# Kernel optimization log

Measured on AMD Instinct MI355X. Metric: run time of the kernel, lower is better.

## Reference

```python
import jax, jax.numpy as jnp
import numpy as np

HEADS = 8
NEG = -1e9
EPS = 1e-9


def setup_inputs() -> dict:
    key = jax.random.key(0)
    ks = jax.random.split(key, 24)
    N, D, E = 2048, 512, 64
    s = 0.02
    inp = {
        "xyz": jax.random.normal(ks[0], (N, 3), jnp.float32),
        "str_feat": jax.random.normal(ks[1], (N, D), jnp.float32),
        "esm_feat": jax.random.normal(ks[2], (N, E), jnp.float32),
        "y_hat": jax.random.uniform(ks[3], (N, 1), jnp.float32),
        "distance_mask": jax.random.randint(ks[4], (N, N), 0, 2, jnp.int32),
        "t": jnp.ones((1,), jnp.float32),
        "band_width": jnp.ones((1,), jnp.float32),
        "max_iter": 5,
        # main projections (torch Linear layout: y = x @ W.T + b)
        "Wq": jax.random.normal(ks[5], (D, D), jnp.float32) * s,
        "bq": jnp.zeros((D,), jnp.float32),
        "Wk": jax.random.normal(ks[6], (D, D), jnp.float32) * s,
        "bk": jnp.zeros((D,), jnp.float32),
        "Wv": jax.random.normal(ks[7], (D, D), jnp.float32) * s,
        "bv": jnp.zeros((D,), jnp.float32),
        "Wo": jax.random.normal(ks[8], (D, D), jnp.float32) * s,
        "bo": jnp.zeros((D,), jnp.float32),
        # esm projections (computed in the original forward but unused downstream)
        "Weq": jax.random.normal(ks[9], (E, E), jnp.float32) * s,
        "beq": jnp.zeros((E,), jnp.float32),
        "Wek": jax.random.normal(ks[10], (E, E), jnp.float32) * s,
        "bek": jnp.zeros((E,), jnp.float32),
        "Wev": jax.random.normal(ks[11], (E, E), jnp.float32) * s,
        "bev": jnp.zeros((E,), jnp.float32),
        "Weo": jax.random.normal(ks[12], (E, E), jnp.float32) * s,
        "beo": jnp.zeros((E,), jnp.float32),
    }
    return inp


def reference(xyz, str_feat, esm_feat, y_hat, distance_mask, t, band_width, max_iter,
              Wq, bq, Wk, bk, Wv, bv, Wo, bo,
              Weq, beq, Wek, bek, Wev, bev, Weo, beo):
    N, D = str_feat.shape
    h = HEADS
    dh = D // h

    q = str_feat @ Wq.T + bq
    k = str_feat @ Wk.T + bk
    v = str_feat @ Wv.T + bv
    # esm projections: computed in the original forward but never used (dead code; DCE'd under jit)
    _esm_q = esm_feat @ Weq.T + beq
    _esm_k = esm_feat @ Wek.T + bek
    _esm_v = esm_feat @ Wev.T + bev

    # [h, N, dh]
    qh = q.reshape(N, h, dh).transpose(1, 0, 2)
    kh = k.reshape(N, h, dh).transpose(1, 0, 2)
    vh = v.reshape(N, h, dh).transpose(1, 0, 2)

    scores = jnp.einsum('hnd,hmd->hnm', qh, kh) / jnp.sqrt(jnp.asarray(dh, qh.dtype))
    mask = (distance_mask > 0)[None]              # [1, N, N]
    yw = y_hat[:, 0][None, :]                     # [1, N] per-target weight
    inv_two_bw2 = 1.0 / (2.0 * band_width[0] ** 2)
    temp = t[0]

    def step(carry, _):
        xyz_c, _x = carry
        # squared pairwise distances via the expanded form (avoids [N,N,3])
        sq = jnp.sum(xyz_c * xyz_c, axis=-1)
        d2 = sq[:, None] + sq[None, :] - 2.0 * (xyz_c @ xyz_c.T)
        kern = jnp.exp(-d2 * inv_two_bw2)          # [N, N] band-width kernel
        logits = scores / temp + jnp.log(kern * yw + EPS)[None]
        logits = jnp.where(mask, logits, NEG)
        attn = jax.nn.softmax(logits, axis=-1)     # [h, N, N]
        xyz_new = jnp.einsum('nm,md->nd', attn.mean(0), xyz_c)  # mean-shift step
        x_new = jnp.einsum('hnm,hmd->hnd', attn, vh)            # [h, N, dh]
        return (xyz_new, x_new), None

    (xyz_out, xh), _ = jax.lax.scan(step, (xyz, jnp.zeros_like(vh)), None, length=max_iter)
    x = xh.transpose(1, 0, 2).reshape(N, D)
    out = x @ Wo.T + bo
    return xyz_out, out
```

## Files before the change

kernel.cpp:

```cpp
#include <hip/hip_runtime.h>


typedef __attribute__((ext_vector_type(8))) short bf16x8;
typedef __attribute__((ext_vector_type(4))) float f32x4;

__device__ __forceinline__ unsigned short f2bf(float f) {
    unsigned int u = __float_as_uint(f);
    u += 0x7fff + ((u >> 16) & 1);
    return (unsigned short)(u >> 16);
}
__device__ __forceinline__ float bf2f(unsigned short u) {
    return __uint_as_float((unsigned int)u << 16);
}

union EU { bf16x8 v; unsigned short u[8]; };

__global__ __launch_bounds__(256)
void conv_all(const float* __restrict__ strf,
              const float* __restrict__ Wq, const float* __restrict__ Wk,
              const float* __restrict__ Wv,
              unsigned short* __restrict__ sA, unsigned short* __restrict__ sW)
{
    const long base = (long)(blockIdx.x * 256 + threadIdx.x) * 8;
    const float* src;
    unsigned short* dst;
    if (base < 1048576) {
        src = strf + base; dst = sA + base;
    } else {
        const long rel = base - 1048576;
        const int seg = (int)(rel >> 18);
        const long off = rel & 262143;
        src = (seg == 0 ? Wq : (seg == 1 ? Wk : Wv)) + off;
        dst = sW + (long)seg * 262144 + off;
    }
    float4 a = *reinterpret_cast<const float4*>(src);
    float4 b = *reinterpret_cast<const float4*>(src + 4);
    EU o;
    o.u[0] = f2bf(a.x); o.u[1] = f2bf(a.y); o.u[2] = f2bf(a.z); o.u[3] = f2bf(a.w);
    o.u[4] = f2bf(b.x); o.u[5] = f2bf(b.y); o.u[6] = f2bf(b.z); o.u[7] = f2bf(b.w);
    *reinterpret_cast<bf16x8*>(dst) = o.v;
}

__global__ __launch_bounds__(256)
void qkv_mfma(const unsigned short* __restrict__ sA,
              const unsigned short* __restrict__ sW,
              const float* __restrict__ bq, const float* __restrict__ bk,
              const float* __restrict__ bv,
              unsigned short* __restrict__ qh, unsigned short* __restrict__ kh,
              unsigned short* __restrict__ vT)
{
    const int z  = blockIdx.z;
    const int bx = blockIdx.x;
    const int by = blockIdx.y;
    const int tid = threadIdx.x;
    const int wv = tid >> 6;
    const int lane = tid & 63;
    const int row  = lane & 15;
    const int koct = (lane >> 4) * 8;
    const int n0 = bx * 64;

    const unsigned short* Ap = sA + (long)(n0 + wv * 16 + row) * 512;
    const unsigned short* Bp = sW + (long)z * 262144 + (long)(by * 64 + row) * 512;

    f32x4 acc[4] = {};
#pragma unroll
    for (int k0 = 0; k0 < 512; k0 += 32) {
        bf16x8 a = *reinterpret_cast<const bf16x8*>(Ap + k0 + koct);
#pragma unroll
        for (int t = 0; t < 4; t++) {
            bf16x8 b = *reinterpret_cast<const bf16x8*>(Bp + (long)(t * 16) * 512 + k0 + koct);
            acc[t] = __builtin_amdgcn_mfma_f32_16x16x32_bf16(a, b, acc[t], 0, 0, 0);
        }
    }

    if (z == 2) {
        const int rbase = n0 + wv * 16 + (lane >> 4) * 4;
#pragma unroll
        for (int t = 0; t < 4; t++) {
            const int d = by * 64 + t * 16 + (lane & 15);
            const float bb = bv[d];
            ushort4 o;
            o.x = f2bf(acc[t][0] + bb); o.y = f2bf(acc[t][1] + bb);
            o.z = f2bf(acc[t][2] + bb); o.w = f2bf(acc[t][3] + bb);
            *reinterpret_cast<ushort4*>(vT + (long)d * 2048 + rbase) = o;
        }
        return;
    }

    __shared__ float ls[64][68];
    const int lrb = wv * 16 + (lane >> 4) * 4;
    const int lcb = lane & 15;
#pragma unroll
    for (int t = 0; t < 4; t++)
#pragma unroll
        for (int r = 0; r < 4; r++)
            ls[lrb + r][t * 16 + lcb] = acc[t][r];
    __syncthreads();

    const float* bias = (z == 0) ? bq : bk;
    unsigned short* dst = (z == 0) ? qh : kh;
    const int r2 = tid >> 2;
    const int c2 = (tid & 3) * 16;
    float sv[16];
#pragma unroll
    for (int j = 0; j < 4; j++) {
        float4 s = *reinterpret_cast<const float4*>(&ls[r2][c2 + j * 4]);
        float4 bb = *reinterpret_cast<const float4*>(bias + by * 64 + c2 + j * 4);
        sv[j*4+0] = s.x + bb.x; sv[j*4+1] = s.y + bb.y;
        sv[j*4+2] = s.z + bb.z; sv[j*4+3] = s.w + bb.w;
    }
    EU o0, o1;
#pragma unroll
    for (int j = 0; j < 8; j++) { o0.u[j] = f2bf(sv[j]); o1.u[j] = f2bf(sv[8 + j]); }
    unsigned short* dp = dst + (long)(n0 + r2) * 512 + by * 64 + c2;
    *reinterpret_cast<bf16x8*>(dp)     = o0.v;
    *reinterpret_cast<bf16x8*>(dp + 8) = o1.v;
}

__global__ __launch_bounds__(256)
void scores_mfma(const unsigned short* __restrict__ qh,
                 const unsigned short* __restrict__ kh,
                 const int* __restrict__ dmask,
                 const float* __restrict__ tptr,
                 unsigned short* __restrict__ Ebf)
{
    const int h  = blockIdx.z;
    const int m0 = blockIdx.x * 128;
    const int n0 = blockIdx.y * 64;
    const int tid = threadIdx.x;
    const int wv = tid >> 6;
    const int lane = tid & 63;
    const float scale = 1.0f / (8.0f * tptr[0]);

    const int row  = lane & 15;
    const int koct = (lane >> 4) * 8;
    const unsigned short* Aq = qh + (long)(n0 + wv * 16 + row) * 512 + h * 64;
    const unsigned short* Bk = kh + (long)(m0 + row) * 512 + h * 64;

    f32x4 acc[8] = {};
#pragma unroll
    for (int k0 = 0; k0 < 64; k0 += 32) {
        bf16x8 a = *reinterpret_cast<const bf16x8*>(Aq + k0 + koct);
#pragma unroll
        for (int t = 0; t < 8; t++) {
            bf16x8 b = *reinterpret_cast<const bf16x8*>(Bk + (long)(t * 16) * 512 + k0 + koct);
            acc[t] = __builtin_amdgcn_mfma_f32_16x16x32_bf16(a, b, acc[t], 0, 0, 0);
        }
    }

    __shared__ float ls[64][68];
    const int lrb = wv * 16 + (lane >> 4) * 4;
    const int lcb = lane & 15;
    const int r2 = tid >> 2;
    const int c2 = (tid & 3) * 16;
    const int gn = n0 + r2;

#pragma unroll
    for (int half = 0; half < 2; half++) {
#pragma unroll
        for (int t = 0; t < 4; t++)
#pragma unroll
            for (int r = 0; r < 4; r++)
                ls[lrb + r][t * 16 + lcb] = acc[half * 4 + t][r];
        __syncthreads();

        const int mcol = m0 + half * 64 + c2;
        const int* mp = dmask + (long)gn * 2048 + mcol;
        int4 mk0 = reinterpret_cast<const int4*>(mp)[0];
        int4 mk1 = reinterpret_cast<const int4*>(mp)[1];
        int4 mk2 = reinterpret_cast<const int4*>(mp)[2];
        int4 mk3 = reinterpret_cast<const int4*>(mp)[3];
        int mk[16] = {mk0.x, mk0.y, mk0.z, mk0.w, mk1.x, mk1.y, mk1.z, mk1.w,
                      mk2.x, mk2.y, mk2.z, mk2.w, mk3.x, mk3.y, mk3.z, mk3.w};
        float4 s0 = *reinterpret_cast<const float4*>(&ls[r2][c2 + 0]);
        float4 s1 = *reinterpret_cast<const float4*>(&ls[r2][c2 + 4]);
        float4 s2 = *reinterpret_cast<const float4*>(&ls[r2][c2 + 8]);
        float4 s3 = *reinterpret_cast<const float4*>(&ls[r2][c2 + 12]);
        float sv[16] = {s0.x, s0.y, s0.z, s0.w, s1.x, s1.y, s1.z, s1.w,
                        s2.x, s2.y, s2.z, s2.w, s3.x, s3.y, s3.z, s3.w};
        EU o0, o1;
#pragma unroll
        for (int j = 0; j < 8; j++)
            o0.u[j] = (mk[j] > 0) ? f2bf(__expf(sv[j] * scale)) : (unsigned short)0;
#pragma unroll
        for (int j = 0; j < 8; j++)
            o1.u[j] = (mk[8 + j] > 0) ? f2bf(__expf(sv[8 + j] * scale)) : (unsigned short)0;
        unsigned short* ep = Ebf + (long)gn * 16384 + h * 2048 + mcol;
        *reinterpret_cast<bf16x8*>(ep)     = o0.v;
        *reinterpret_cast<bf16x8*>(ep + 8) = o1.v;
        __syncthreads();
    }
}

__global__ __launch_bounds__(256)
void ms_iter(const unsigned short* __restrict__ Ebf,
             const float* __restrict__ xyz_src,
             float* __restrict__ xyz_dst,
             const float* __restrict__ y_hat,
             const float* __restrict__ bwp,
             unsigned short* __restrict__ attn_out,
             int write_attn)
{
    const int n = blockIdx.x;
    const int tid = threadIdx.x;
    const int lane = tid & 63;
    const int wave = tid >> 6;
    const int m0 = tid * 8;

    __shared__ float red[64];

    const float bw = bwp[0];
    const float c2k = 1.0f / (2.0f * bw * bw);

    const float xn = xyz_src[n * 3 + 0];
    const float yn = xyz_src[n * 3 + 1];
    const float zn = xyz_src[n * 3 + 2];
    const float sqn = xn * xn + yn * yn + zn * zn;

    float mx[8], my[8], mz[8];
    {
        const float4* xp = reinterpret_cast<const float4*>(xyz_src + (long)m0 * 3);
        float4 a = xp[0], b = xp[1], c = xp[2], d = xp[3], e = xp[4], f = xp[5];
        mx[0]=a.x; my[0]=a.y; mz[0]=a.z;  mx[1]=a.w; my[1]=b.x; mz[1]=b.y;
        mx[2]=b.z; my[2]=b.w; mz[2]=c.x;  mx[3]=c.y; my[3]=c.z; mz[3]=c.w;
        mx[4]=d.x; my[4]=d.y; mz[4]=d.z;  mx[5]=d.w; my[5]=e.x; mz[5]=e.y;
        mx[6]=e.z; my[6]=e.w; mz[6]=f.x;  mx[7]=f.y; my[7]=f.z; mz[7]=f.w;
    }
    float4 yh0 = *reinterpret_cast<const float4*>(y_hat + m0);
    float4 yh1 = *reinterpret_cast<const float4*>(y_hat + m0 + 4);
    float yh[8] = {yh0.x, yh0.y, yh0.z, yh0.w, yh1.x, yh1.y, yh1.z, yh1.w};

    float g[8];
#pragma unroll
    for (int j = 0; j < 8; j++) {
        const float d2 = sqn + (mx[j]*mx[j] + my[j]*my[j] + mz[j]*mz[j])
                       - 2.0f * (xn*mx[j] + yn*my[j] + zn*mz[j]);
        g[j] = __expf(-d2 * c2k) * yh[j] + 1e-9f;
    }

    const unsigned short* Ep = Ebf + (long)n * 16384 + m0;
    EU E[8];
#pragma unroll
    for (int h = 0; h < 8; h++)
        E[h].v = *reinterpret_cast<const bf16x8*>(Ep + h * 2048);

    float z[8];
#pragma unroll
    for (int h = 0; h < 8; h++) {
        float zz = 0.f;
#pragma unroll
        for (int j = 0; j < 8; j++) zz += bf2f(E[h].u[j]) * g[j];
        z[h] = zz;
    }

#pragma unroll
    for (int h = 0; h < 8; h++) {
        float v = z[h];
#pragma unroll
        for (int off = 32; off > 0; off >>= 1) v += __shfl_down(v, off, 64);
        if (lane == 0) red[wave * 8 + h] = v;
    }
    __syncthreads();
    if (tid < 8) {
        const float s = red[tid] + red[8 + tid] + red[16 + tid] + red[24 + tid];
        red[32 + tid] = 1.0f / s;
    }
    __syncthreads();
    float invz[8];
#pragma unroll
    for (int h = 0; h < 8; h++) invz[h] = red[32 + h];
    __syncthreads();

    float ax = 0.f, ay = 0.f, az = 0.f;
#pragma unroll
    for (int j = 0; j < 8; j++) {
        float w = 0.f;
#pragma unroll
        for (int h = 0; h < 8; h++) w += bf2f(E[h].u[j]) * invz[h];
        w *= 0.125f * g[j];
        ax += w * mx[j]; ay += w * my[j]; az += w * mz[j];
    }
    if (write_attn) {
        unsigned short* ap = attn_out + (long)n * 16384 + m0;
#pragma unroll
        for (int h = 0; h < 8; h++) {
            EU o;
#pragma unroll
            for (int j = 0; j < 8; j++)
                o.u[j] = f2bf(bf2f(E[h].u[j]) * g[j] * invz[h]);
            *reinterpret_cast<bf16x8*>(ap + h * 2048) = o.v;
        }
    }

    float v3[3] = {ax, ay, az};
#pragma unroll
    for (int c = 0; c < 3; c++) {
        float v = v3[c];
#pragma unroll
        for (int off = 32; off > 0; off >>= 1) v += __shfl_down(v, off, 64);
        if (lane == 0) red[c * 4 + wave] = v;
    }
    __syncthreads();
    if (tid < 3) {
        xyz_dst[n * 3 + tid] = red[tid * 4 + 0] + red[tid * 4 + 1] +
                               red[tid * 4 + 2] + red[tid * 4 + 3];
    }
}

__global__ __launch_bounds__(256)
void av_mfma(const unsigned short* __restrict__ attn,
             const unsigned short* __restrict__ vT,
             float* __restrict__ xb)
{
    const int h  = blockIdx.z;
    const int s  = blockIdx.y;
    const int bx = blockIdx.x;
    const int wv = threadIdx.x >> 6;
    const int lane = threadIdx.x & 63;
    const int n0 = bx * 64 + wv * 16;
    const int kc = s * 512;

    const int mrow = lane & 15;
    const int koct = (lane >> 4) * 8;

    const unsigned short* Ab = attn + (long)(n0 + mrow) * 16384 + h * 2048;
    const unsigned short* Bb = vT + ((long)h * 64 + mrow) * 2048;

    f32x4 acc[4] = {};
    for (int k0 = kc; k0 < kc + 512; k0 += 32) {
        bf16x8 a = *reinterpret_cast<const bf16x8*>(Ab + k0 + koct);
#pragma unroll
        for (int t = 0; t < 4; t++) {
            bf16x8 b = *reinterpret_cast<const bf16x8*>(Bb + (long)(t * 16) * 2048 + k0 + koct);
            acc[t] = __builtin_amdgcn_mfma_f32_16x16x32_bf16(a, b, acc[t], 0, 0, 0);
        }
    }

    const int rbase = n0 + (lane >> 4) * 4;
    const int dcol = lane & 15;
#pragma unroll
    for (int t = 0; t < 4; t++)
#pragma unroll
        for (int r = 0; r < 4; r++)
            atomicAdd(&xb[(long)(rbase + r) * 512 + h * 64 + t * 16 + dcol], acc[t][r]);
}

__global__ __launch_bounds__(256)
void gemm_nt(const float* __restrict__ A,
             const float* __restrict__ B,
             const float* __restrict__ bias,
             float* __restrict__ C)
{
    __shared__ float As[16][68];
    __shared__ float Bs[16][68];

    const int tid = threadIdx.x;
    const int i0 = blockIdx.x * 64;
    const int j0 = blockIdx.y * 64;
    const int tx = tid & 15, ty = tid >> 4;
    const int lr = tid >> 2;
    const int lc = (tid & 3) << 2;

    float acc[4][4] = {};

    for (int k0 = 0; k0 < 512; k0 += 16) {
        float4 av = *reinterpret_cast<const float4*>(A + (long)(i0 + lr) * 512 + (k0 + lc));
        float4 bv = *reinterpret_cast<const float4*>(B + (long)(j0 + lr) * 512 + (k0 + lc));
        As[lc + 0][lr] = av.x; As[lc + 1][lr] = av.y; As[lc + 2][lr] = av.z; As[lc + 3][lr] = av.w;
        Bs[lc + 0][lr] = bv.x; Bs[lc + 1][lr] = bv.y; Bs[lc + 2][lr] = bv.z; Bs[lc + 3][lr] = bv.w;
        __syncthreads();
#pragma unroll
        for (int kk = 0; kk < 16; kk++) {
            float4 a = *reinterpret_cast<const float4*>(&As[kk][ty << 2]);
            float4 b = *reinterpret_cast<const float4*>(&Bs[kk][tx << 2]);
            float ar[4] = {a.x, a.y, a.z, a.w};
            float br[4] = {b.x, b.y, b.z, b.w};
#pragma unroll
            for (int p = 0; p < 4; p++)
#pragma unroll
                for (int q = 0; q < 4; q++)
                    acc[p][q] += ar[p] * br[q];
        }
        __syncthreads();
    }

#pragma unroll
    for (int p = 0; p < 4; p++) {
        const int row = i0 + (ty << 2) + p;
        const int col = j0 + (tx << 2);
        float4 o;
        o.x = acc[p][0] + bias[col + 0];
        o.y = acc[p][1] + bias[col + 1];
        o.z = acc[p][2] + bias[col + 2];
        o.w = acc[p][3] + bias[col + 3];
        *reinterpret_cast<float4*>(C + (long)row * 512 + col) = o;
    }
}

extern "C" void kernel_launch(void* const* d_in, const int* in_sizes, int n_in,
                              void* d_out, int out_size, void* d_ws, size_t ws_size,
                              hipStream_t stream)
{
    (void)in_sizes; (void)n_in; (void)out_size; (void)ws_size;

    const float* xyz   = (const float*)d_in[0];
    const float* strf  = (const float*)d_in[1];
    const float* yhat  = (const float*)d_in[3];
    const int*   dmask = (const int*)d_in[4];
    const float* tptr  = (const float*)d_in[5];
    const float* bwptr = (const float*)d_in[6];
    const float* Wq = (const float*)d_in[8];
    const float* bq = (const float*)d_in[9];
    const float* Wk = (const float*)d_in[10];
    const float* bk = (const float*)d_in[11];
    const float* Wv = (const float*)d_in[12];
    const float* bv = (const float*)d_in[13];
    const float* Wo = (const float*)d_in[14];
    const float* bo = (const float*)d_in[15];
    float* outp = (float*)d_out;

    char* wsb = (char*)d_ws;
    float* xb            = (float*)(wsb);
    unsigned short* sA   = (unsigned short*)(wsb + (4L << 20));
    unsigned short* sW   = (unsigned short*)(wsb + (6L << 20));
    unsigned short* qh   = (unsigned short*)(wsb + (8L << 20));
    unsigned short* kh   = (unsigned short*)(wsb + (10L << 20));
    unsigned short* vT   = (unsigned short*)(wsb + (12L << 20));
    float* xyzA          = (float*)(wsb + (14L << 20));
    float* xyzB          = xyzA + 8192;
    unsigned short* Ebf  = (unsigned short*)(wsb + (16L << 20));

    dim3 blk(256, 1, 1);

    conv_all<<<dim3(896), blk, 0, stream>>>(strf, Wq, Wk, Wv, sA, sW);
    qkv_mfma<<<dim3(32, 8, 3), blk, 0, stream>>>(sA, sW, bq, bk, bv, qh, kh, vT);

    scores_mfma<<<dim3(16, 32, 8), blk, 0, stream>>>(qh, kh, dmask, tptr, Ebf);

    const float* src = xyz;
    float* dsts[5] = {xyzA, xyzB, xyzA, xyzB, outp};
    for (int it = 0; it < 5; it++) {
        ms_iter<<<dim3(2048), blk, 0, stream>>>(Ebf, src, dsts[it], yhat, bwptr,
                                                Ebf, it == 4 ? 1 : 0);
        src = dsts[it];
    }

    hipMemsetAsync(xb, 0, 2048L * 512 * sizeof(float), stream);
    av_mfma<<<dim3(32, 4, 8), blk, 0, stream>>>(Ebf, vT, xb);

    gemm_nt<<<dim3(32, 8, 1), blk, 0, stream>>>(xb, Wo, bo, outp + 6144);
}
```

Before: 372.2 us.

## Pack distance mask to bytes once and streamline scores epilogue with per-wave LDS

The conversion kernel now also packs the int32 distance mask into a byte mask, so scores_mfma reads 4x less mask data across its 8 head passes. The scores epilogue drops the block-wide LDS staging and two barriers: each wave writes exp'd bf16 values to its own LDS tile, then applies the byte mask and stores 32 contiguous elements per lane. The E loads in ms_iter are hoisted to the top and made nontemporal, and av_mfma's attention loads are also nontemporal. In exchange, an extra 4MB pass over the mask is added to the conversion launch and extra workspace is used.

```diff
diff --git a/kernel.cpp b/kernel.cpp
--- a/kernel.cpp
+++ b/kernel.cpp
@@ -2,7 +2,9 @@
 
 
 typedef __attribute__((ext_vector_type(8))) short bf16x8;
+typedef __attribute__((ext_vector_type(4))) short bf16x4;
 typedef __attribute__((ext_vector_type(4))) float f32x4;
+typedef __attribute__((ext_vector_type(4))) int   i32x4;
 
 __device__ __forceinline__ unsigned short f2bf(float f) {
     unsigned int u = __float_as_uint(f);
@@ -13,15 +15,29 @@
     return __uint_as_float((unsigned int)u << 16);
 }
 
-union EU { bf16x8 v; unsigned short u[8]; };
+union EU  { bf16x8 v; i32x4 i; unsigned short u[8]; };
+union EU4 { bf16x4 v; unsigned short u[4]; };
 
 __global__ __launch_bounds__(256)
 void conv_all(const float* __restrict__ strf,
               const float* __restrict__ Wq, const float* __restrict__ Wk,
-              const float* __restrict__ Wv,
-              unsigned short* __restrict__ sA, unsigned short* __restrict__ sW)
+              const float* __restrict__ Wv, const int* __restrict__ dmask,
+              unsigned short* __restrict__ sA, unsigned short* __restrict__ sW,
+              unsigned char* __restrict__ mby)
 {
     const long base = (long)(blockIdx.x * 256 + threadIdx.x) * 8;
+    if (base >= 1048576 + 786432) {
+        const long rel = base - (1048576 + 786432);
+        int4 a = *reinterpret_cast<const int4*>(dmask + rel);
+        int4 b = *reinterpret_cast<const int4*>(dmask + rel + 4);
+        unsigned long long p = 0;
+        p |= (a.x > 0) ? 0x01ULL : 0;  p |= (a.y > 0) ? 0x0100ULL : 0;
+        p |= (a.z > 0) ? 0x010000ULL : 0;  p |= (a.w > 0) ? 0x01000000ULL : 0;
+        p |= (b.x > 0) ? 0x0100000000ULL : 0;  p |= (b.y > 0) ? 0x010000000000ULL : 0;
+        p |= (b.z > 0) ? 0x01000000000000ULL : 0;  p |= (b.w > 0) ? 0x0100000000000000ULL : 0;
+        *reinterpret_cast<unsigned long long*>(mby + rel) = p;
+        return;
+    }
     const float* src;
     unsigned short* dst;
     if (base < 1048576) {
@@ -120,7 +136,7 @@
 __global__ __launch_bounds__(256)
 void scores_mfma(const unsigned short* __restrict__ qh,
                  const unsigned short* __restrict__ kh,
-                 const int* __restrict__ dmask,
+                 const unsigned char* __restrict__ mby,
                  const float* __restrict__ tptr,
                  unsigned short* __restrict__ Ebf)
 {
@@ -148,48 +164,39 @@
         }
     }
 
-    __shared__ float ls[64][68];
-    const int lrb = wv * 16 + (lane >> 4) * 4;
-    const int lcb = lane & 15;
-    const int r2 = tid >> 2;
-    const int c2 = (tid & 3) * 16;
-    const int gn = n0 + r2;
-
-#pragma unroll
-    for (int half = 0; half < 2; half++) {
-#pragma unroll
-        for (int t = 0; t < 4; t++)
-#pragma unroll
-            for (int r = 0; r < 4; r++)
-                ls[lrb + r][t * 16 + lcb] = acc[half * 4 + t][r];
-        __syncthreads();
-
-        const int mcol = m0 + half * 64 + c2;
-        const int* mp = dmask + (long)gn * 2048 + mcol;
-        int4 mk0 = reinterpret_cast<const int4*>(mp)[0];
-        int4 mk1 = reinterpret_cast<const int4*>(mp)[1];
-        int4 mk2 = reinterpret_cast<const int4*>(mp)[2];
-        int4 mk3 = reinterpret_cast<const int4*>(mp)[3];
-        int mk[16] = {mk0.x, mk0.y, mk0.z, mk0.w, mk1.x, mk1.y, mk1.z, mk1.w,
-                      mk2.x, mk2.y, mk2.z, mk2.w, mk3.x, mk3.y, mk3.z, mk3.w};
-        float4 s0 = *reinterpret_cast<const float4*>(&ls[r2][c2 + 0]);
-        float4 s1 = *reinterpret_cast<const float4*>(&ls[r2][c2 + 4]);
-        float4 s2 = *reinterpret_cast<const float4*>(&ls[r2][c2 + 8]);
-        float4 s3 = *reinterpret_cast<const float4*>(&ls[r2][c2 + 12]);
-        float sv[16] = {s0.x, s0.y, s0.z, s0.w, s1.x, s1.y, s1.z, s1.w,
-                        s2.x, s2.y, s2.z, s2.w, s3.x, s3.y, s3.z, s3.w};
-        EU o0, o1;
-#pragma unroll
-        for (int j = 0; j < 8; j++)
-            o0.u[j] = (mk[j] > 0) ? f2bf(__expf(sv[j] * scale)) : (unsigned short)0;
-#pragma unroll
-        for (int j = 0; j < 8; j++)
-            o1.u[j] = (mk[8 + j] > 0) ? f2bf(__expf(sv[8 + j] * scale)) : (unsigned short)0;
-        unsigned short* ep = Ebf + (long)gn * 16384 + h * 2048 + mcol;
-        *reinterpret_cast<bf16x8*>(ep)     = o0.v;
-        *reinterpret_cast<bf16x8*>(ep + 8) = o1.v;
-        __syncthreads();
-    }
+    __shared__ unsigned short lsb[4][16][140];
+    const int rr = (lane >> 4) * 4;
+    const int cc = lane & 15;
+#pragma unroll
+    for (int t = 0; t < 8; t++)
+#pragma unroll
+        for (int r = 0; r < 4; r++)
+            lsb[wv][rr + r][t * 16 + cc] = f2bf(__expf(acc[t][r] * scale));
+
+    const int rr2 = lane >> 2;
+    const int c32 = (lane & 3) * 32;
+    const int gn  = n0 + wv * 16 + rr2;
+
+    EU4 ev[8];
+#pragma unroll
+    for (int j = 0; j < 8; j++)
+        ev[j].v = *reinterpret_cast<const bf16x4*>(&lsb[wv][rr2][c32 + 4 * j]);
+
+    union MB { uint4 q; unsigned char b[16]; } mb0, mb1;
+    const unsigned char* mrow = mby + (long)gn * 2048 + m0 + c32;
+    mb0.q = *reinterpret_cast<const uint4*>(mrow);
+    mb1.q = *reinterpret_cast<const uint4*>(mrow + 16);
+
+    EU o[4];
+#pragma unroll
+    for (int e = 0; e < 32; e++) {
+        const unsigned char mk = (e < 16) ? mb0.b[e] : mb1.b[e - 16];
+        o[e >> 3].u[e & 7] = mk ? ev[e >> 2].u[e & 3] : (unsigned short)0;
+    }
+    unsigned short* ep = Ebf + (long)gn * 16384 + h * 2048 + m0 + c32;
+#pragma unroll
+    for (int t = 0; t < 4; t++)
+        *reinterpret_cast<bf16x8*>(ep + t * 8) = o[t].v;
 }
 
 __global__ __launch_bounds__(256)
@@ -208,6 +215,12 @@
     const int m0 = tid * 8;
 
     __shared__ float red[64];
+
+    EU E[8];
+    const i32x4* Epv = reinterpret_cast<const i32x4*>(Ebf + (long)n * 16384 + m0);
+#pragma unroll
+    for (int h = 0; h < 8; h++)
+        E[h].i = __builtin_nontemporal_load(Epv + h * 256);
 
     const float bw = bwp[0];
     const float c2k = 1.0f / (2.0f * bw * bw);
@@ -238,12 +251,6 @@
         g[j] = __expf(-d2 * c2k) * yh[j] + 1e-9f;
     }
 
-    const unsigned short* Ep = Ebf + (long)n * 16384 + m0;
-    EU E[8];
-#pragma unroll
-    for (int h = 0; h < 8; h++)
-        E[h].v = *reinterpret_cast<const bf16x8*>(Ep + h * 2048);
-
     float z[8];
 #pragma unroll
     for (int h = 0; h < 8; h++) {
@@ -328,11 +335,12 @@
 
     f32x4 acc[4] = {};
     for (int k0 = kc; k0 < kc + 512; k0 += 32) {
-        bf16x8 a = *reinterpret_cast<const bf16x8*>(Ab + k0 + koct);
+        EU au;
+        au.i = __builtin_nontemporal_load(reinterpret_cast<const i32x4*>(Ab + k0 + koct));
 #pragma unroll
         for (int t = 0; t < 4; t++) {
             bf16x8 b = *reinterpret_cast<const bf16x8*>(Bb + (long)(t * 16) * 2048 + k0 + koct);
-            acc[t] = __builtin_amdgcn_mfma_f32_16x16x32_bf16(a, b, acc[t], 0, 0, 0);
+            acc[t] = __builtin_amdgcn_mfma_f32_16x16x32_bf16(au.v, b, acc[t], 0, 0, 0);
         }
     }
 
@@ -429,13 +437,14 @@
     float* xyzA          = (float*)(wsb + (14L << 20));
     float* xyzB          = xyzA + 8192;
     unsigned short* Ebf  = (unsigned short*)(wsb + (16L << 20));
+    unsigned char* mby   = (unsigned char*)(wsb + (80L << 20));
 
     dim3 blk(256, 1, 1);
 
-    conv_all<<<dim3(896), blk, 0, stream>>>(strf, Wq, Wk, Wv, sA, sW);
+    conv_all<<<dim3(2944), blk, 0, stream>>>(strf, Wq, Wk, Wv, dmask, sA, sW, mby);
     qkv_mfma<<<dim3(32, 8, 3), blk, 0, stream>>>(sA, sW, bq, bk, bv, qh, kh, vT);
 
-    scores_mfma<<<dim3(16, 32, 8), blk, 0, stream>>>(qh, kh, dmask, tptr, Ebf);
+    scores_mfma<<<dim3(16, 32, 8), blk, 0, stream>>>(qh, kh, mby, tptr, Ebf);
 
     const float* src = xyz;
     float* dsts[5] = {xyzA, xyzB, xyzA, xyzB, outp};
```

New measurement: 387.0 us. 4.0% more time.
